# Optimization experiments

Measured on AMD Instinct MI355X. Metric: run time of the kernel, lower is better.

The kernel has to match this reference:

```python
import jax, jax.numpy as jnp
import numpy as np

N_NODES = 100000
N_EDGES = 1600000
D = 64


def _sage_conv(x, src, dst, W_l, W_r, b):
    # PyG SAGEConv (aggr='mean'): out_i = W_l @ mean_{j in N(i)} x_j + W_r @ x_i + b
    n = x.shape[0]
    msgs = x[src]  # [E, D] gather of source-node features
    agg = jax.ops.segment_sum(msgs, dst, num_segments=n)  # [N, D]
    cnt = jax.ops.segment_sum(jnp.ones((src.shape[0],), x.dtype), dst, num_segments=n)
    mean = agg / jnp.maximum(cnt, 1.0)[:, None]
    return mean @ W_l.T + x @ W_r.T + b


def setup_inputs() -> dict:
    key = jax.random.key(0)
    ks = jax.random.split(key, 8)
    s = 1.0 / np.sqrt(D)
    x = jax.random.normal(ks[0], (N_NODES, D), dtype=jnp.float32)
    edge_index = jax.random.randint(ks[1], (2, N_EDGES), 0, N_NODES, dtype=jnp.int64)
    return {
        "x": x,
        "edge_index": edge_index,
        "W1_l": jax.random.normal(ks[2], (D, D), dtype=jnp.float32) * s,
        "W1_r": jax.random.normal(ks[3], (D, D), dtype=jnp.float32) * s,
        "b1": jnp.zeros((D,), dtype=jnp.float32),
        "W2_l": jax.random.normal(ks[4], (D, D), dtype=jnp.float32) * s,
        "W2_r": jax.random.normal(ks[5], (D, D), dtype=jnp.float32) * s,
        "b2": jnp.zeros((D,), dtype=jnp.float32),
    }


def reference(x, edge_index, W1_l, W1_r, b1, W2_l, W2_r, b2):
    src, dst = edge_index[0], edge_index[1]
    h = _sage_conv(x, src, dst, W1_l, W1_r, b1)
    h = jax.nn.relu(h)
    out = _sage_conv(h, src, dst, W2_l, W2_r, b2)
    return out
```

## Files before the change

### kernel.cpp

```cpp
#include <hip/hip_runtime.h>

#define D 64
#define BSH2 6
#define BN2 (1 << BSH2)
#define RSH 9
#define RN (1 << RSH)
#define NR_MAX 256
#define RCAPSH 14
#define RCAP (1 << RCAPSH)
#define SPR_MAX 2048
#define SIDX_MAX (SPR_MAX + 3 * BN2)

typedef __attribute__((ext_vector_type(8))) short bf16x8;
typedef __attribute__((ext_vector_type(4))) float f32x4;

__device__ __forceinline__ unsigned int f2bf_rne(float f) {
    unsigned int b = __float_as_uint(f);
    return (b + 0x7fffu + ((b >> 16) & 1u)) >> 16;
}
__device__ __forceinline__ unsigned int pack_bf(float lo, float hi) {
    return f2bf_rne(lo) | (f2bf_rne(hi) << 16);
}
__device__ __forceinline__ float bflo(unsigned int u) { return __uint_as_float(u << 16); }
__device__ __forceinline__ float bfhi(unsigned int u) { return __uint_as_float(u & 0xffff0000u); }

__global__ void cast_kernel(const float4* __restrict__ xin, uint2* __restrict__ xb, int n4,
                            int* __restrict__ cnt, int nz) {
    int gid = blockIdx.x * blockDim.x + threadIdx.x;
    if (gid < nz) cnt[gid] = 0;
    int stride = gridDim.x * blockDim.x;
    for (int i = gid; i < n4; i += stride) {
        float4 v = xin[i];
        uint2 o;
        o.x = pack_bf(v.x, v.y);
        o.y = pack_bf(v.z, v.w);
        xb[i] = o;
    }
}

__global__ __launch_bounds__(256) void binscatter_kernel(
    const int* __restrict__ src, const int* __restrict__ dst,
    int* __restrict__ cnt, unsigned int* __restrict__ pairs,
    int E, int NR, int CE) {
    __shared__ int lh[NR_MAX];
    __shared__ int lbase[NR_MAX];
    for (int k = threadIdx.x; k < NR; k += 256) lh[k] = 0;
    __syncthreads();
    int b = blockIdx.x;
    int beg = b * CE, end = min(beg + CE, E);
    for (int e = beg + threadIdx.x; e < end; e += 256)
        atomicAdd(&lh[dst[e] >> RSH], 1);
    __syncthreads();
    for (int k = threadIdx.x; k < NR; k += 256) {
        int c = lh[k];
        if (c) lbase[k] = (k << RCAPSH) + atomicAdd(&cnt[k], c);
        lh[k] = 0;
    }
    __syncthreads();
    for (int e = beg + threadIdx.x; e < end; e += 256) {
        int d = dst[e];
        int k = d >> RSH;
        int r = atomicAdd(&lh[k], 1);
        pairs[lbase[k] + r] = (unsigned int)src[e] | ((unsigned int)(d & (RN - 1)) << 17);
    }
}

__global__ __launch_bounds__(256) void fused_layer_kernel(
    const unsigned int* __restrict__ xin, const unsigned int* __restrict__ pairs,
    const int* __restrict__ cnt,
    const float* __restrict__ Wl, const float* __restrict__ Wr,
    const float* __restrict__ bias,
    float* __restrict__ outf, unsigned int* __restrict__ outb,
    int N, int NR, int relu) {
    __shared__ uint4 smean[BN2][8];
    __shared__ int sidx[SIDX_MAX];
    __shared__ int lcnt[BN2];
    __shared__ int lbase[BN2];
    __shared__ int lcur[BN2];
    __shared__ int sscan[BN2];
    __shared__ int scnt0;

    unsigned int* spr = (unsigned int*)&smean[0][0];

    int x = blockIdx.x & 7;
    int j = blockIdx.x >> 3;
    int region = ((j >> 3) << 3) | x;
    int sub = j & 7;
    if (region >= NR) return;
    int node0 = (region << RSH) + (sub << BSH2);
    if (node0 >= N) return;

    int tid = threadIdx.x;
    int wave = tid >> 6;
    int lane = tid & 63;

    if (tid == 0) scnt0 = 0;
    if (tid < BN2) lcnt[tid] = 0;
    __syncthreads();
    int cR = min(cnt[region], RCAP);
    int rb = region << RCAPSH;
    for (int i = tid; i < cR; i += 256) {
        unsigned int rec = pairs[rb + i];
        if (((rec >> 23) & 7u) == (unsigned int)sub) {
            int p = atomicAdd(&scnt0, 1);
            if (p < SPR_MAX) {
                spr[p] = rec;
                atomicAdd(&lcnt[(rec >> 17) & (BN2 - 1)], 1);
            }
        }
    }
    __syncthreads();
    int cntk = min(scnt0, SPR_MAX);
    int deg = (tid < BN2) ? lcnt[tid] : 0;
    int ps  = (deg + 3) & ~3;
    if (tid < BN2) sscan[tid] = ps;
    __syncthreads();
    for (int off = 1; off < BN2; off <<= 1) {
        int t = (tid < BN2 && tid >= off) ? sscan[tid - off] : 0;
        __syncthreads();
        if (tid < BN2) sscan[tid] += t;
        __syncthreads();
    }
    if (tid < BN2) {
        int base = sscan[tid] - ps;
        lbase[tid] = base;
        lcur[tid] = base;
    }
    __syncthreads();
    for (int i = tid; i < cntk; i += 256) {
        unsigned int rec = spr[i];
        int jn = (rec >> 17) & (BN2 - 1);
        int pos = atomicAdd(&lcur[jn], 1);
        sidx[pos] = (int)(rec & 0x1FFFFu);
    }
    __syncthreads();

    int q  = lane >> 3;
    int fl = lane & 7;
    for (int o = 0; o < 2; ++o) {
        int nl = (wave << 4) + (o << 3) + q;
        int beg = lbase[nl];
        int dg  = lcnt[nl];
        int end = beg + dg;
        float s0 = 0.f, s1 = 0.f, s2 = 0.f, s3 = 0.f;
        float s4 = 0.f, s5 = 0.f, s6 = 0.f, s7 = 0.f;
        int jj = beg;
        for (; jj + 4 <= end; jj += 4) {
            int4 iv = *(const int4*)(sidx + jj);
            uint4 u0 = *(const uint4*)(xin + iv.x * 32 + fl * 4);
            uint4 u1 = *(const uint4*)(xin + iv.y * 32 + fl * 4);
            uint4 u2 = *(const uint4*)(xin + iv.z * 32 + fl * 4);
            uint4 u3 = *(const uint4*)(xin + iv.w * 32 + fl * 4);
            s0 += bflo(u0.x) + bflo(u1.x) + bflo(u2.x) + bflo(u3.x);
            s1 += bfhi(u0.x) + bfhi(u1.x) + bfhi(u2.x) + bfhi(u3.x);
            s2 += bflo(u0.y) + bflo(u1.y) + bflo(u2.y) + bflo(u3.y);
            s3 += bfhi(u0.y) + bfhi(u1.y) + bfhi(u2.y) + bfhi(u3.y);
            s4 += bflo(u0.z) + bflo(u1.z) + bflo(u2.z) + bflo(u3.z);
            s5 += bfhi(u0.z) + bfhi(u1.z) + bfhi(u2.z) + bfhi(u3.z);
            s6 += bflo(u0.w) + bflo(u1.w) + bflo(u2.w) + bflo(u3.w);
            s7 += bfhi(u0.w) + bfhi(u1.w) + bfhi(u2.w) + bfhi(u3.w);
        }
        for (; jj < end; ++jj) {
            uint4 u = *(const uint4*)(xin + sidx[jj] * 32 + fl * 4);
            s0 += bflo(u.x); s1 += bfhi(u.x);
            s2 += bflo(u.y); s3 += bfhi(u.y);
            s4 += bflo(u.z); s5 += bfhi(u.z);
            s6 += bflo(u.w); s7 += bfhi(u.w);
        }
        float inv = 1.0f / fmaxf((float)dg, 1.0f);
        uint4 ov;
        ov.x = pack_bf(s0 * inv, s1 * inv);
        ov.y = pack_bf(s2 * inv, s3 * inv);
        ov.z = pack_bf(s4 * inv, s5 * inv);
        ov.w = pack_bf(s6 * inv, s7 * inv);
        smean[nl][fl ^ (nl & 7)] = ov;
    }

    int lm   = lane & 15;
    int quad = lane >> 4;
    int f_a  = (wave << 4) + lm;
    bf16x8 wh[4], wlo[4];
#pragma unroll
    for (int s = 0; s < 4; ++s) {
        int k8 = s * 32 + quad * 8;
        const float* Wsrc = (k8 < 64) ? Wl : Wr;
        const float* p = Wsrc + f_a * 64 + (k8 & 63);
        float4 w0 = *(const float4*)p;
        float4 w1 = *(const float4*)(p + 4);
        float w[8] = {w0.x, w0.y, w0.z, w0.w, w1.x, w1.y, w1.z, w1.w};
        bf16x8 h, l;
#pragma unroll
        for (int jj = 0; jj < 8; ++jj) {
            unsigned int hb = f2bf_rne(w[jj]);
            float hf = __uint_as_float(hb << 16);
            unsigned int lb = f2bf_rne(w[jj] - hf);
            h[jj] = (short)hb;
            l[jj] = (short)lb;
        }
        wh[s] = h;
        wlo[s] = l;
    }

    __syncthreads();

    f32x4 acc[4];
#pragma unroll
    for (int nt = 0; nt < 4; ++nt) acc[nt] = (f32x4){0.f, 0.f, 0.f, 0.f};

#pragma unroll
    for (int nt = 0; nt < 4; ++nt) {
        int nl = nt * 16 + lm;
        int node = node0 + nl;
        bool v = node < N;
        const unsigned int* xrow = xin + (long long)node * 32;
#pragma unroll
        for (int s = 0; s < 2; ++s) {
            union { uint4 u4; bf16x8 v8; } cv;
            cv.u4 = smean[nl][(s * 4 + quad) ^ (lm & 7)];
            acc[nt] = __builtin_amdgcn_mfma_f32_16x16x32_bf16(wh[s],  cv.v8, acc[nt], 0, 0, 0);
            acc[nt] = __builtin_amdgcn_mfma_f32_16x16x32_bf16(wlo[s], cv.v8, acc[nt], 0, 0, 0);
        }
#pragma unroll
        for (int s = 2; s < 4; ++s) {
            uint4 u = make_uint4(0u, 0u, 0u, 0u);
            if (v) u = *(const uint4*)(xrow + ((s & 1) << 4) + (quad << 2));
            union { uint4 u4; bf16x8 v8; } cv;
            cv.u4 = u;
            acc[nt] = __builtin_amdgcn_mfma_f32_16x16x32_bf16(wh[s],  cv.v8, acc[nt], 0, 0, 0);
            acc[nt] = __builtin_amdgcn_mfma_f32_16x16x32_bf16(wlo[s], cv.v8, acc[nt], 0, 0, 0);
        }
    }

    int fb = (wave << 4) + quad * 4;
    float4 bv = *(const float4*)(bias + fb);
#pragma unroll
    for (int nt = 0; nt < 4; ++nt) {
        int node = node0 + nt * 16 + lm;
        if (node >= N) continue;
        float r0 = acc[nt][0] + bv.x;
        float r1 = acc[nt][1] + bv.y;
        float r2 = acc[nt][2] + bv.z;
        float r3 = acc[nt][3] + bv.w;
        if (relu) {
            r0 = fmaxf(r0, 0.f); r1 = fmaxf(r1, 0.f);
            r2 = fmaxf(r2, 0.f); r3 = fmaxf(r3, 0.f);
        }
        if (outf) *(float4*)(outf + (long long)node * D + fb) = make_float4(r0, r1, r2, r3);
        if (outb) *(uint2*)(outb + (long long)node * 32 + (fb >> 1)) =
                      make_uint2(pack_bf(r0, r1), pack_bf(r2, r3));
    }
}

extern "C" void kernel_launch(void* const* d_in, const int* in_sizes, int n_in,
                              void* d_out, int out_size, void* d_ws, size_t ws_size,
                              hipStream_t stream) {
    const float* x   = (const float*)d_in[0];
    const int* ei    = (const int*)d_in[1];
    const float* W1l = (const float*)d_in[2];
    const float* W1r = (const float*)d_in[3];
    const float* b1  = (const float*)d_in[4];
    const float* W2l = (const float*)d_in[5];
    const float* W2r = (const float*)d_in[6];
    const float* b2  = (const float*)d_in[7];

    const int E = in_sizes[1] / 2;
    const int N = in_sizes[0] / D;
    const int* src  = ei;
    const int* dstp = ei + E;
    const int NR = (N + RN - 1) >> RSH;
    const int G1 = 512;
    const int CE = (E + G1 - 1) / G1;
    const int G2 = 64 * ((NR + 7) >> 3);

    char* ws = (char*)d_ws;
    size_t off = 0;
    auto alloc = [&](size_t bytes) { void* p = ws + off; off = (off + bytes + 255) & ~(size_t)255; return p; };
    int* cnt            = (int*)alloc((size_t)NR * 4);
    unsigned int* pairs = (unsigned int*)alloc(((size_t)(NR + 1) << RCAPSH) * 4);
    unsigned int* xb    = (unsigned int*)alloc((size_t)N * 32 * 4);
    unsigned int* hb    = (unsigned int*)alloc((size_t)N * 32 * 4);

    float* out = (float*)d_out;

    cast_kernel<<<2048, 256, 0, stream>>>((const float4*)x, (uint2*)xb, N * 16, cnt, NR);

    binscatter_kernel<<<G1, 256, 0, stream>>>(src, dstp, cnt, pairs, E, NR, CE);

    fused_layer_kernel<<<G2, 256, 0, stream>>>(xb, pairs, cnt, W1l, W1r, b1,
                                               nullptr, hb, N, NR, 1);
    fused_layer_kernel<<<G2, 256, 0, stream>>>(hb, pairs, cnt, W2l, W2r, b2,
                                               out, nullptr, N, NR, 0);
}
```

Measured before the change: 251.6 us.

## Add rebin pass to pre-split region edge lists into per-block sub-bins

A new rebin kernel counting-sorts each 512-node region's edge records into eight 64-node sub-bins once, writing a compact per-block list and count. Both fused layer kernels then read only their own sub-bin instead of scanning the whole region's records and keeping one eighth. This removes the eightfold redundant pair reads and shared-memory atomic filtering in each layer. The cost is one extra launch plus an extra global write and read of the edge list. It also drops the old swizzled block-to-region mapping and caps each region at a smaller staging size (RSTAGE).

```diff
diff --git a/kernel.cpp b/kernel.cpp
--- a/kernel.cpp
+++ b/kernel.cpp
@@ -8,7 +8,10 @@
 #define NR_MAX 256
 #define RCAPSH 14
 #define RCAP (1 << RCAPSH)
-#define SPR_MAX 2048
+#define RSTAGE 12288
+#define FCAPSH 11
+#define FCAP (1 << FCAPSH)
+#define SPR_MAX FCAP
 #define SIDX_MAX (SPR_MAX + 3 * BN2)
 
 typedef __attribute__((ext_vector_type(8))) short bf16x8;
@@ -65,52 +68,92 @@
     }
 }
 
+__global__ __launch_bounds__(256) void rebin_kernel(
+    const unsigned int* __restrict__ pairs, const int* __restrict__ cnt,
+    unsigned int* __restrict__ pairs2, int* __restrict__ cnt2, int NR) {
+    __shared__ unsigned int srt[RSTAGE];
+    __shared__ int cm[2048];
+    __shared__ int sblk[256];
+    __shared__ int sbase[9];
+    int r = blockIdx.x;
+    int tid = threadIdx.x;
+    int cR = min(cnt[r], RSTAGE);
+    int rb = r << RCAPSH;
+
+    int myc[8] = {0, 0, 0, 0, 0, 0, 0, 0};
+    for (int i = tid; i < cR; i += 256)
+        myc[(pairs[rb + i] >> 23) & 7u]++;
+#pragma unroll
+    for (int s = 0; s < 8; ++s) cm[s * 256 + tid] = myc[s];
+    __syncthreads();
+    int loc[8];
+    int sum = 0;
+#pragma unroll
+    for (int k = 0; k < 8; ++k) { int v = cm[tid * 8 + k]; loc[k] = sum; sum += v; }
+    sblk[tid] = sum;
+    __syncthreads();
+    for (int off = 1; off < 256; off <<= 1) {
+        int t = (tid >= off) ? sblk[tid - off] : 0;
+        __syncthreads();
+        sblk[tid] += t;
+        __syncthreads();
+    }
+    int ebase = sblk[tid] - sum;
+#pragma unroll
+    for (int k = 0; k < 8; ++k) cm[tid * 8 + k] = ebase + loc[k];
+    __syncthreads();
+    if (tid < 8) sbase[tid] = cm[tid * 256];
+    if (tid == 0) sbase[8] = sblk[255];
+    int off8[8];
+#pragma unroll
+    for (int s = 0; s < 8; ++s) off8[s] = cm[s * 256 + tid];
+    for (int i = tid; i < cR; i += 256) {
+        unsigned int rec = pairs[rb + i];
+        int s = (rec >> 23) & 7u;
+        srt[off8[s]++] = rec & 0x7FFFFFu;
+    }
+    __syncthreads();
+#pragma unroll
+    for (int s = 0; s < 8; ++s) {
+        int cs = sbase[s];
+        int n = min(sbase[s + 1] - cs, FCAP);
+        unsigned int* dp = pairs2 + ((size_t)((r << 3) + s) << FCAPSH);
+        for (int i = tid; i < n; i += 256) dp[i] = srt[cs + i];
+        if (tid == 0) cnt2[(r << 3) + s] = n;
+    }
+}
+
 __global__ __launch_bounds__(256) void fused_layer_kernel(
-    const unsigned int* __restrict__ xin, const unsigned int* __restrict__ pairs,
-    const int* __restrict__ cnt,
+    const unsigned int* __restrict__ xin, const unsigned int* __restrict__ pairs2,
+    const int* __restrict__ cnt2,
     const float* __restrict__ Wl, const float* __restrict__ Wr,
     const float* __restrict__ bias,
-    float* __restrict__ outf, unsigned int* __restrict__ outb,
-    int N, int NR, int relu) {
+    float* __restrict__ outf, unsigned int* __restrict__ outb, int N, int relu) {
     __shared__ uint4 smean[BN2][8];
     __shared__ int sidx[SIDX_MAX];
     __shared__ int lcnt[BN2];
     __shared__ int lbase[BN2];
     __shared__ int lcur[BN2];
     __shared__ int sscan[BN2];
-    __shared__ int scnt0;
 
     unsigned int* spr = (unsigned int*)&smean[0][0];
-
-    int x = blockIdx.x & 7;
-    int j = blockIdx.x >> 3;
-    int region = ((j >> 3) << 3) | x;
-    int sub = j & 7;
-    if (region >= NR) return;
-    int node0 = (region << RSH) + (sub << BSH2);
-    if (node0 >= N) return;
 
     int tid = threadIdx.x;
     int wave = tid >> 6;
     int lane = tid & 63;
-
-    if (tid == 0) scnt0 = 0;
+    int b = blockIdx.x;
+    int node0 = b << BSH2;
+
+    int cntk = min(cnt2[b], SPR_MAX);
     if (tid < BN2) lcnt[tid] = 0;
     __syncthreads();
-    int cR = min(cnt[region], RCAP);
-    int rb = region << RCAPSH;
-    for (int i = tid; i < cR; i += 256) {
-        unsigned int rec = pairs[rb + i];
-        if (((rec >> 23) & 7u) == (unsigned int)sub) {
-            int p = atomicAdd(&scnt0, 1);
-            if (p < SPR_MAX) {
-                spr[p] = rec;
-                atomicAdd(&lcnt[(rec >> 17) & (BN2 - 1)], 1);
-            }
-        }
-    }
-    __syncthreads();
-    int cntk = min(scnt0, SPR_MAX);
+    long long rbeg = (long long)b << FCAPSH;
+    for (int i = tid; i < cntk; i += 256) {
+        unsigned int rec = pairs2[rbeg + i];
+        spr[i] = rec;
+        atomicAdd(&lcnt[(rec >> 17) & (BN2 - 1)], 1);
+    }
+    __syncthreads();
     int deg = (tid < BN2) ? lcnt[tid] : 0;
     int ps  = (deg + 3) & ~3;
     if (tid < BN2) sscan[tid] = ps;
@@ -129,8 +172,8 @@
     __syncthreads();
     for (int i = tid; i < cntk; i += 256) {
         unsigned int rec = spr[i];
-        int jn = (rec >> 17) & (BN2 - 1);
-        int pos = atomicAdd(&lcur[jn], 1);
+        int j = (rec >> 17) & (BN2 - 1);
+        int pos = atomicAdd(&lcur[j], 1);
         sidx[pos] = (int)(rec & 0x1FFFFu);
     }
     __syncthreads();
@@ -144,9 +187,9 @@
         int end = beg + dg;
         float s0 = 0.f, s1 = 0.f, s2 = 0.f, s3 = 0.f;
         float s4 = 0.f, s5 = 0.f, s6 = 0.f, s7 = 0.f;
-        int jj = beg;
-        for (; jj + 4 <= end; jj += 4) {
-            int4 iv = *(const int4*)(sidx + jj);
+        int j = beg;
+        for (; j + 4 <= end; j += 4) {
+            int4 iv = *(const int4*)(sidx + j);
             uint4 u0 = *(const uint4*)(xin + iv.x * 32 + fl * 4);
             uint4 u1 = *(const uint4*)(xin + iv.y * 32 + fl * 4);
             uint4 u2 = *(const uint4*)(xin + iv.z * 32 + fl * 4);
@@ -160,8 +203,8 @@
             s6 += bflo(u0.w) + bflo(u1.w) + bflo(u2.w) + bflo(u3.w);
             s7 += bfhi(u0.w) + bfhi(u1.w) + bfhi(u2.w) + bfhi(u3.w);
         }
-        for (; jj < end; ++jj) {
-            uint4 u = *(const uint4*)(xin + sidx[jj] * 32 + fl * 4);
+        for (; j < end; ++j) {
+            uint4 u = *(const uint4*)(xin + sidx[j] * 32 + fl * 4);
             s0 += bflo(u.x); s1 += bfhi(u.x);
             s2 += bflo(u.y); s3 += bfhi(u.y);
             s4 += bflo(u.z); s5 += bfhi(u.z);
@@ -267,18 +310,20 @@
     const int N = in_sizes[0] / D;
     const int* src  = ei;
     const int* dstp = ei + E;
-    const int NR = (N + RN - 1) >> RSH;
+    const int NR  = (N + RN - 1) >> RSH;
+    const int NBF = (N + BN2 - 1) >> BSH2;
     const int G1 = 512;
     const int CE = (E + G1 - 1) / G1;
-    const int G2 = 64 * ((NR + 7) >> 3);
 
     char* ws = (char*)d_ws;
     size_t off = 0;
     auto alloc = [&](size_t bytes) { void* p = ws + off; off = (off + bytes + 255) & ~(size_t)255; return p; };
-    int* cnt            = (int*)alloc((size_t)NR * 4);
-    unsigned int* pairs = (unsigned int*)alloc(((size_t)(NR + 1) << RCAPSH) * 4);
-    unsigned int* xb    = (unsigned int*)alloc((size_t)N * 32 * 4);
-    unsigned int* hb    = (unsigned int*)alloc((size_t)N * 32 * 4);
+    int* cnt             = (int*)alloc((size_t)NR * 4);
+    int* cnt2            = (int*)alloc((size_t)(NR * 8) * 4);
+    unsigned int* pairs  = (unsigned int*)alloc(((size_t)(NR + 1) << RCAPSH) * 4);
+    unsigned int* pairs2 = (unsigned int*)alloc(((size_t)(NR * 8 + 8) << FCAPSH) * 4);
+    unsigned int* xb     = (unsigned int*)alloc((size_t)N * 32 * 4);
+    unsigned int* hb     = (unsigned int*)alloc((size_t)N * 32 * 4);
 
     float* out = (float*)d_out;
 
@@ -286,8 +331,10 @@
 
     binscatter_kernel<<<G1, 256, 0, stream>>>(src, dstp, cnt, pairs, E, NR, CE);
 
-    fused_layer_kernel<<<G2, 256, 0, stream>>>(xb, pairs, cnt, W1l, W1r, b1,
-                                               nullptr, hb, N, NR, 1);
-    fused_layer_kernel<<<G2, 256, 0, stream>>>(hb, pairs, cnt, W2l, W2r, b2,
-                                               out, nullptr, N, NR, 0);
-}
+    rebin_kernel<<<NR, 256, 0, stream>>>(pairs, cnt, pairs2, cnt2, NR);
+
+    fused_layer_kernel<<<NBF, 256, 0, stream>>>(xb, pairs2, cnt2, W1l, W1r, b1,
+                                                nullptr, hb, N, 1);
+    fused_layer_kernel<<<NBF, 256, 0, stream>>>(hb, pairs2, cnt2, W2l, W2r, b2,
+                                                out, nullptr, N, 0);
+}
```

New measurement: 233.5 us. -7.2%, faster.
